# Performance work log

Measured on AMD Instinct MI355X. Metric: run time of the kernel, lower is better.

The kernel has to match this reference:

```python
import jax, jax.numpy as jnp
import numpy as np

B, N, F_IN, F_OUT = 32, 1024, 64, 64
ALPHA = 0.2  # LeakyReLU negative slope


def setup_inputs() -> dict:
    key = jax.random.key(0)
    k1, k2, k3, k4 = jax.random.split(key, 4)
    node_features = jax.random.normal(k1, (B, N, F_IN), dtype=jnp.float32)
    adjacency = jax.random.uniform(k2, (B, N, N)) > 0.5
    adjacency = adjacency | jnp.eye(N, dtype=bool)[None]  # self-loops: no all-masked row
    # xavier_uniform-scale params (normal with matching std is fine for a reference)
    W = jax.random.normal(k3, (F_IN, F_OUT), dtype=jnp.float32) * (2.0 / (F_IN + F_OUT)) ** 0.5
    a = jax.random.normal(k4, (2 * F_OUT, 1), dtype=jnp.float32) * (2.0 / (2 * F_OUT + 1)) ** 0.5
    return {"node_features": node_features, "adjacency": adjacency, "W": W, "a": a}


def reference(node_features, adjacency, W, a):
    # h = X W : (B, N, F_OUT)
    h = node_features @ W
    # a^T [h_i || h_j] = h_i . a1 + h_j . a2  (exact decomposition of the concat score)
    a1 = a[:F_OUT, 0]
    a2 = a[F_OUT:, 0]
    f1 = jnp.einsum('bnf,f->bn', h, a1)  # (B, N)
    f2 = jnp.einsum('bnf,f->bn', h, a2)  # (B, N)
    e = jax.nn.leaky_relu(f1[:, :, None] + f2[:, None, :], negative_slope=ALPHA)  # (B,N,N)
    e = jnp.where(adjacency, e, -jnp.inf)
    attention = jax.nn.softmax(e, axis=-1)  # masked softmax over neighbors j
    h_prime = jnp.einsum('bij,bjf->bif', attention, h)  # (B, N, F_OUT)
    return jax.nn.elu(h_prime)  # concat=True branch
```

## Files before the change

### kernel.cpp

```cpp
#include <hip/hip_runtime.h>
#include <hip/hip_bf16.h>


#define B_  32
#define N_  1024
#define F_  64

typedef __attribute__((ext_vector_type(8))) short  short8;
typedef __attribute__((ext_vector_type(4))) float  floatx4;

__device__ __forceinline__ short f2bf(float x) {
    unsigned u = __float_as_uint(x);
    u += 0x7fff + ((u >> 16) & 1);
    return (short)(u >> 16);
}

__global__ __launch_bounds__(256) void gat_prep(
    const float* __restrict__ nf, const float* __restrict__ W, const float* __restrict__ a,
    float* __restrict__ f1, float* __restrict__ f2, short* __restrict__ h_swz)
{
    const int wave = threadIdx.x >> 6;
    const int lane = threadIdx.x & 63;
    const long long row0 = (long long)blockIdx.x * 16 + wave * 4;

    const float* nf0 = nf + row0 * F_;
    float acc0 = 0.f, acc1 = 0.f, acc2 = 0.f, acc3 = 0.f;
    #pragma unroll 8
    for (int k = 0; k < F_; ++k) {
        float wk = W[k * F_ + lane];
        acc0 = fmaf(nf0[k],          wk, acc0);
        acc1 = fmaf(nf0[F_ + k],     wk, acc1);
        acc2 = fmaf(nf0[2 * F_ + k], wk, acc2);
        acc3 = fmaf(nf0[3 * F_ + k], wk, acc3);
    }
    const float a1 = a[lane], a2 = a[F_ + lane];

    float accs[4] = {acc0, acc1, acc2, acc3};
    #pragma unroll
    for (int r = 0; r < 4; ++r) {
        float v  = accs[r];
        float s1 = v * a1, s2 = v * a2;
        #pragma unroll
        for (int off = 32; off >= 1; off >>= 1) {
            s1 += __shfl_xor(s1, off, 64);
            s2 += __shfl_xor(s2, off, 64);
        }
        long long row = row0 + r;
        if (lane == 0) { f1[row] = s1; f2[row] = s2; }
        int jl = (int)(row & (N_ - 1));
        int k  = jl & 31;
        int n  = lane & 15, fg = lane >> 4;
        int lp = n | ((k >> 3) << 4), e = k & 7;
        long long gc = row >> 5;
        h_swz[(gc * 4 + fg) * 512 + lp * 8 + e] = f2bf(v);
    }
}

__global__ __launch_bounds__(256, 8) void gat_attn(
    const int* __restrict__ adj, const float* __restrict__ f1g, const float* __restrict__ f2g,
    const short* __restrict__ h_swz, float* __restrict__ out)
{
    __shared__ float part[4][64][17];
    __shared__ float srow[4][16];

    const int wave = threadIdx.x >> 6;
    const int lane = threadIdx.x & 63;
    const int b  = blockIdx.x >> 6;
    const int ig = blockIdx.x & 63;
    const int i_base = ig * 16;
    const int iw = lane & 15;
    const int kg = lane >> 4;
    const int i  = i_base + iw;
    const int j0 = wave * 256;

    const float f1i = f1g[b * N_ + i];
    const int*   adjrow = adj + ((long long)b * N_ + i) * N_ + j0 + kg * 8;
    const float* f2b    = f2g + b * N_ + j0 + kg * 8;
    const short* hb     = h_swz + (long long)b * 65536 + wave * (8 * 2048) + lane * 8;

    floatx4 acc0 = {0.f,0.f,0.f,0.f}, acc1 = {0.f,0.f,0.f,0.f};
    floatx4 acc2 = {0.f,0.f,0.f,0.f}, acc3 = {0.f,0.f,0.f,0.f};
    float s_lane = 0.f;

    for (int jc = 0; jc < 8; ++jc) {
        int4 aA = *(const int4*)(adjrow + jc * 32);
        int4 aB = *(const int4*)(adjrow + jc * 32 + 4);
        floatx4 fA = *(const floatx4*)(f2b + jc * 32);
        floatx4 fB = *(const floatx4*)(f2b + jc * 32 + 4);

        const short* hc = hb + jc * 2048;
        short8 b0 = *(const short8*)(hc);
        short8 b1 = *(const short8*)(hc + 512);
        short8 b2 = *(const short8*)(hc + 1024);
        short8 b3 = *(const short8*)(hc + 1536);

        short8 afrag;
        {
            int   am[4] = {aA.x, aA.y, aA.z, aA.w};
            #pragma unroll
            for (int e = 0; e < 4; ++e) {
                float x  = f1i + fA[e];
                x        = fmaxf(x, 0.2f * x);
                float pe = am[e] ? __expf(x) : 0.f;
                s_lane  += pe;
                afrag[e] = f2bf(pe);
            }
        }
        {
            int   am[4] = {aB.x, aB.y, aB.z, aB.w};
            #pragma unroll
            for (int e = 0; e < 4; ++e) {
                float x  = f1i + fB[e];
                x        = fmaxf(x, 0.2f * x);
                float pe = am[e] ? __expf(x) : 0.f;
                s_lane  += pe;
                afrag[e + 4] = f2bf(pe);
            }
        }

        acc0 = __builtin_amdgcn_mfma_f32_16x16x32_bf16(afrag, b0, acc0, 0, 0, 0);
        acc1 = __builtin_amdgcn_mfma_f32_16x16x32_bf16(afrag, b1, acc1, 0, 0, 0);
        acc2 = __builtin_amdgcn_mfma_f32_16x16x32_bf16(afrag, b2, acc2, 0, 0, 0);
        acc3 = __builtin_amdgcn_mfma_f32_16x16x32_bf16(afrag, b3, acc3, 0, 0, 0);
    }

    s_lane += __shfl_xor(s_lane, 16, 64);
    s_lane += __shfl_xor(s_lane, 32, 64);
    if (lane < 16) srow[wave][lane] = s_lane;

    floatx4 accs[4] = {acc0, acc1, acc2, acc3};
    #pragma unroll
    for (int fg = 0; fg < 4; ++fg)
        #pragma unroll
        for (int r = 0; r < 4; ++r)
            part[wave][lane][fg * 4 + r] = accs[fg][r];
    __syncthreads();

    const int fg = wave;
    float* orow = out + ((long long)b * N_ + i_base) * F_;
    #pragma unroll
    for (int r = 0; r < 4; ++r) {
        const int idx  = fg * 4 + r;
        const int rloc = kg * 4 + r;
        float tot  = part[0][lane][idx] + part[1][lane][idx]
                   + part[2][lane][idx] + part[3][lane][idx];
        float sden = srow[0][rloc] + srow[1][rloc] + srow[2][rloc] + srow[3][rloc];
        float v = tot / sden;
        v = v > 0.f ? v : (__expf(v) - 1.f);
        orow[(long long)rloc * F_ + fg * 16 + iw] = v;
    }
}

extern "C" void kernel_launch(void* const* d_in, const int* in_sizes, int n_in,
                              void* d_out, int out_size, void* d_ws, size_t ws_size,
                              hipStream_t stream) {
    const float* nf  = (const float*)d_in[0];
    const int*   adj = (const int*)d_in[1];
    const float* W   = (const float*)d_in[2];
    const float* a   = (const float*)d_in[3];
    float* out = (float*)d_out;

    char* ws = (char*)d_ws;
    float* f1    = (float*)ws;
    float* f2    = (float*)(ws + 131072);
    short* h_swz = (short*)(ws + 262144);

    hipLaunchKernelGGL(gat_prep, dim3(B_ * N_ / 16), dim3(256), 0, stream,
                       nf, W, a, f1, f2, h_swz);
    hipLaunchKernelGGL(gat_attn, dim3(B_ * (N_ / 16)), dim3(256), 0, stream,
                       adj, f1, f2, h_swz, out);
}
```

Before: 60.69 us.

## Pack adjacency mask into bits in a separate pass before attention

Adds a kernel that compresses the 4-byte-per-entry adjacency mask into a bitmask (one byte per 8 neighbors). The attention kernel then reads one byte per 8 columns instead of two int4 loads. It also relaxes the occupancy hint from 8 to 4 blocks per CU and unrolls the inner loop by 2. The full int mask is still read every call, now by a simpler streaming kernel. The trade-off is an extra launch and an extra write/read of the packed mask, in return for taking the bulk load off the latency-sensitive MFMA loop.

```diff
diff --git a/kernel.cpp b/kernel.cpp
--- a/kernel.cpp
+++ b/kernel.cpp
@@ -13,6 +13,23 @@
     unsigned u = __float_as_uint(x);
     u += 0x7fff + ((u >> 16) & 1);
     return (short)(u >> 16);
+}
+
+__global__ __launch_bounds__(256) void adj2bit(
+    const int* __restrict__ adj, unsigned char* __restrict__ bits)
+{
+    const long long total = (long long)B_ * N_ * N_ / 8;
+    const long long nth   = (long long)gridDim.x * 256;
+    for (long long o = (long long)blockIdx.x * 256 + threadIdx.x; o < total; o += nth) {
+        const int* p = adj + o * 8;
+        int4 v0 = *(const int4*)(p);
+        int4 v1 = *(const int4*)(p + 4);
+        unsigned by = (v0.x != 0)        | ((v0.y != 0) << 1)
+                    | ((v0.z != 0) << 2) | ((v0.w != 0) << 3)
+                    | ((v1.x != 0) << 4) | ((v1.y != 0) << 5)
+                    | ((v1.z != 0) << 6) | ((v1.w != 0) << 7);
+        bits[o] = (unsigned char)by;
+    }
 }
 
 __global__ __launch_bounds__(256) void gat_prep(
@@ -56,9 +73,10 @@
     }
 }
 
-__global__ __launch_bounds__(256, 8) void gat_attn(
-    const int* __restrict__ adj, const float* __restrict__ f1g, const float* __restrict__ f2g,
-    const short* __restrict__ h_swz, float* __restrict__ out)
+__global__ __launch_bounds__(256, 4) void gat_attn(
+    const unsigned char* __restrict__ bits, const float* __restrict__ f1g,
+    const float* __restrict__ f2g, const short* __restrict__ h_swz,
+    float* __restrict__ out)
 {
     __shared__ float part[4][64][17];
     __shared__ float srow[4][16];
@@ -74,17 +92,17 @@
     const int j0 = wave * 256;
 
     const float f1i = f1g[b * N_ + i];
-    const int*   adjrow = adj + ((long long)b * N_ + i) * N_ + j0 + kg * 8;
-    const float* f2b    = f2g + b * N_ + j0 + kg * 8;
-    const short* hb     = h_swz + (long long)b * 65536 + wave * (8 * 2048) + lane * 8;
+    const unsigned char* bitrow = bits + ((long long)b * N_ + i) * (N_ / 8) + wave * 32 + kg;
+    const float* f2b = f2g + b * N_ + j0 + kg * 8;
+    const short* hb  = h_swz + (long long)b * 65536 + wave * 16384 + lane * 8;
 
     floatx4 acc0 = {0.f,0.f,0.f,0.f}, acc1 = {0.f,0.f,0.f,0.f};
     floatx4 acc2 = {0.f,0.f,0.f,0.f}, acc3 = {0.f,0.f,0.f,0.f};
     float s_lane = 0.f;
 
+    #pragma unroll 2
     for (int jc = 0; jc < 8; ++jc) {
-        int4 aA = *(const int4*)(adjrow + jc * 32);
-        int4 aB = *(const int4*)(adjrow + jc * 32 + 4);
+        unsigned m = bitrow[jc * 4];
         floatx4 fA = *(const floatx4*)(f2b + jc * 32);
         floatx4 fB = *(const floatx4*)(f2b + jc * 32 + 4);
 
@@ -95,27 +113,21 @@
         short8 b3 = *(const short8*)(hc + 1536);
 
         short8 afrag;
-        {
-            int   am[4] = {aA.x, aA.y, aA.z, aA.w};
-            #pragma unroll
-            for (int e = 0; e < 4; ++e) {
-                float x  = f1i + fA[e];
-                x        = fmaxf(x, 0.2f * x);
-                float pe = am[e] ? __expf(x) : 0.f;
-                s_lane  += pe;
-                afrag[e] = f2bf(pe);
-            }
+        #pragma unroll
+        for (int e = 0; e < 4; ++e) {
+            float x  = f1i + fA[e];
+            x        = fmaxf(x, 0.2f * x);
+            float pe = ((m >> e) & 1) ? __expf(x) : 0.f;
+            s_lane  += pe;
+            afrag[e] = f2bf(pe);
         }
-        {
-            int   am[4] = {aB.x, aB.y, aB.z, aB.w};
-            #pragma unroll
-            for (int e = 0; e < 4; ++e) {
-                float x  = f1i + fB[e];
-                x        = fmaxf(x, 0.2f * x);
-                float pe = am[e] ? __expf(x) : 0.f;
-                s_lane  += pe;
-                afrag[e + 4] = f2bf(pe);
-            }
+        #pragma unroll
+        for (int e = 0; e < 4; ++e) {
+            float x  = f1i + fB[e];
+            x        = fmaxf(x, 0.2f * x);
+            float pe = ((m >> (e + 4)) & 1) ? __expf(x) : 0.f;
+            s_lane  += pe;
+            afrag[e + 4] = f2bf(pe);
         }
 
         acc0 = __builtin_amdgcn_mfma_f32_16x16x32_bf16(afrag, b0, acc0, 0, 0, 0);
@@ -164,9 +176,11 @@
     float* f1    = (float*)ws;
     float* f2    = (float*)(ws + 131072);
     short* h_swz = (short*)(ws + 262144);
+    unsigned char* bits = (unsigned char*)(ws + 262144 + 4194304);
 
+    hipLaunchKernelGGL(adj2bit, dim3(2048), dim3(256), 0, stream, adj, bits);
     hipLaunchKernelGGL(gat_prep, dim3(B_ * N_ / 16), dim3(256), 0, stream,
                        nf, W, a, f1, f2, h_swz);
     hipLaunchKernelGGL(gat_attn, dim3(B_ * (N_ / 16)), dim3(256), 0, stream,
-                       adj, f1, f2, h_swz, out);
+                       bits, f1, f2, h_swz, out);
 }
```

New measurement: 74.04 us. 1.22x slower.

## Stage attention probabilities through LDS with coalesced adjacency loads and MFMA row sums

Applied to the files above, without the earlier changes.

The attention kernel now reads adjacency rows in a fully coalesced pattern: each lane loads 4 consecutive ints for each of 16 rows. It computes the masked exp weights and writes them as bf16 into a swizzled LDS tile, which the MFMA loop then reads back as A fragments. The softmax denominator is now computed by an extra MFMA against a ones vector instead of a per-lane sum plus shuffles. This aims to speed up the dominant adjacency read, at the cost of 32KB more LDS per block, lower occupancy (launch bounds drop to 4 blocks per SM), and a denominator summed from bf16-rounded values.

```diff
diff --git a/kernel.cpp b/kernel.cpp
--- a/kernel.cpp
+++ b/kernel.cpp
@@ -7,6 +7,7 @@
 #define F_  64
 
 typedef __attribute__((ext_vector_type(8))) short  short8;
+typedef __attribute__((ext_vector_type(4))) short  short4v;
 typedef __attribute__((ext_vector_type(4))) float  floatx4;
 
 __device__ __forceinline__ short f2bf(float x) {
@@ -56,10 +57,12 @@
     }
 }
 
-__global__ __launch_bounds__(256, 8) void gat_attn(
-    const int* __restrict__ adj, const float* __restrict__ f1g, const float* __restrict__ f2g,
-    const short* __restrict__ h_swz, float* __restrict__ out)
+__global__ __launch_bounds__(256, 4) void gat_attn(
+    const int* __restrict__ adj, const float* __restrict__ f1g,
+    const float* __restrict__ f2g, const short* __restrict__ h_swz,
+    float* __restrict__ outp)
 {
+    __shared__ short Plds[4][16][256];
     __shared__ float part[4][64][17];
     __shared__ float srow[4][16];
 
@@ -70,23 +73,41 @@
     const int i_base = ig * 16;
     const int iw = lane & 15;
     const int kg = lane >> 4;
-    const int i  = i_base + iw;
     const int j0 = wave * 256;
 
-    const float f1i = f1g[b * N_ + i];
-    const int*   adjrow = adj + ((long long)b * N_ + i) * N_ + j0 + kg * 8;
-    const float* f2b    = f2g + b * N_ + j0 + kg * 8;
-    const short* hb     = h_swz + (long long)b * 65536 + wave * (8 * 2048) + lane * 8;
+    const float f1v = f1g[b * N_ + i_base + iw];
+    const floatx4 f2v = *(const floatx4*)(f2g + b * N_ + j0 + lane * 4);
+    const int* adjbase = adj + ((long long)b * N_ + i_base) * N_ + j0 + lane * 4;
+
+    #pragma unroll
+    for (int r = 0; r < 16; ++r) {
+        int4 av = *(const int4*)(adjbase + (long long)r * N_);
+        float f1r = __shfl(f1v, r, 64);
+        int am[4] = {av.x, av.y, av.z, av.w};
+        short4v pk;
+        #pragma unroll
+        for (int e = 0; e < 4; ++e) {
+            float x  = f1r + f2v[e];
+            x        = fmaxf(x, 0.2f * x);
+            float pe = am[e] ? __expf(x) : 0.f;
+            pk[e]    = f2bf(pe);
+        }
+        int g = (lane >> 1) ^ (r & 7);
+        *(short4v*)&Plds[wave][r][g * 8 + (lane & 1) * 4] = pk;
+    }
 
     floatx4 acc0 = {0.f,0.f,0.f,0.f}, acc1 = {0.f,0.f,0.f,0.f};
     floatx4 acc2 = {0.f,0.f,0.f,0.f}, acc3 = {0.f,0.f,0.f,0.f};
-    float s_lane = 0.f;
+    floatx4 acc4 = {0.f,0.f,0.f,0.f};
+    short8 ones;
+    #pragma unroll
+    for (int e = 0; e < 8; ++e) ones[e] = (short)0x3F80;
 
+    const short* hb = h_swz + (long long)b * 65536 + wave * 16384 + lane * 8;
+    #pragma unroll
     for (int jc = 0; jc < 8; ++jc) {
-        int4 aA = *(const int4*)(adjrow + jc * 32);
-        int4 aB = *(const int4*)(adjrow + jc * 32 + 4);
-        floatx4 fA = *(const floatx4*)(f2b + jc * 32);
-        floatx4 fB = *(const floatx4*)(f2b + jc * 32 + 4);
+        int g = (jc * 4 + kg) ^ (iw & 7);
+        short8 af = *(const short8*)&Plds[wave][iw][g * 8];
 
         const short* hc = hb + jc * 2048;
         short8 b0 = *(const short8*)(hc);
@@ -94,39 +115,17 @@
         short8 b2 = *(const short8*)(hc + 1024);
         short8 b3 = *(const short8*)(hc + 1536);
 
-        short8 afrag;
-        {
-            int   am[4] = {aA.x, aA.y, aA.z, aA.w};
-            #pragma unroll
-            for (int e = 0; e < 4; ++e) {
-                float x  = f1i + fA[e];
-                x        = fmaxf(x, 0.2f * x);
-                float pe = am[e] ? __expf(x) : 0.f;
-                s_lane  += pe;
-                afrag[e] = f2bf(pe);
-            }
-        }
-        {
-            int   am[4] = {aB.x, aB.y, aB.z, aB.w};
-            #pragma unroll
-            for (int e = 0; e < 4; ++e) {
-                float x  = f1i + fB[e];
-                x        = fmaxf(x, 0.2f * x);
-                float pe = am[e] ? __expf(x) : 0.f;
-                s_lane  += pe;
-                afrag[e + 4] = f2bf(pe);
-            }
-        }
-
-        acc0 = __builtin_amdgcn_mfma_f32_16x16x32_bf16(afrag, b0, acc0, 0, 0, 0);
-        acc1 = __builtin_amdgcn_mfma_f32_16x16x32_bf16(afrag, b1, acc1, 0, 0, 0);
-        acc2 = __builtin_amdgcn_mfma_f32_16x16x32_bf16(afrag, b2, acc2, 0, 0, 0);
-        acc3 = __builtin_amdgcn_mfma_f32_16x16x32_bf16(afrag, b3, acc3, 0, 0, 0);
+        acc0 = __builtin_amdgcn_mfma_f32_16x16x32_bf16(af, b0, acc0, 0, 0, 0);
+        acc1 = __builtin_amdgcn_mfma_f32_16x16x32_bf16(af, b1, acc1, 0, 0, 0);
+        acc2 = __builtin_amdgcn_mfma_f32_16x16x32_bf16(af, b2, acc2, 0, 0, 0);
+        acc3 = __builtin_amdgcn_mfma_f32_16x16x32_bf16(af, b3, acc3, 0, 0, 0);
+        acc4 = __builtin_amdgcn_mfma_f32_16x16x32_bf16(af, ones, acc4, 0, 0, 0);
     }
 
-    s_lane += __shfl_xor(s_lane, 16, 64);
-    s_lane += __shfl_xor(s_lane, 32, 64);
-    if (lane < 16) srow[wave][lane] = s_lane;
+    if (iw == 0) {
+        #pragma unroll
+        for (int r = 0; r < 4; ++r) srow[wave][kg * 4 + r] = acc4[r];
+    }
 
     floatx4 accs[4] = {acc0, acc1, acc2, acc3};
     #pragma unroll
@@ -137,7 +136,7 @@
     __syncthreads();
 
     const int fg = wave;
-    float* orow = out + ((long long)b * N_ + i_base) * F_;
+    float* orow = outp + ((long long)b * N_ + i_base) * F_;
     #pragma unroll
     for (int r = 0; r < 4; ++r) {
         const int idx  = fg * 4 + r;
```

Result: slower. 64.31 us (+6.0%).
